# Kernel optimization log

Hardware: AMD Instinct MI355X
Metric: run time of the kernel (lower is better)

## Reference

```python
import jax, jax.numpy as jnp
import numpy as np

EMBED_DIM = 1024
NUM_HEADS = 16
HEAD_DIM = EMBED_DIM // NUM_HEADS
B, N = 8, 1024


def setup_inputs() -> dict:
    key = jax.random.key(0)
    k1, k2, k3, k4, k5, k6 = jax.random.split(key, 6)
    scale = 1.0 / np.sqrt(EMBED_DIM)
    return {
        "x": jax.random.normal(k1, (B, N, EMBED_DIM), dtype=jnp.float32),
        "attn_mask": jax.random.normal(k2, (N, N), dtype=jnp.float32) * 0.1,
        "in_proj_weight": jax.random.normal(k3, (3 * EMBED_DIM, EMBED_DIM), dtype=jnp.float32) * scale,
        "in_proj_bias": jax.random.normal(k4, (3 * EMBED_DIM,), dtype=jnp.float32) * 0.02,
        "out_w": jax.random.normal(k5, (EMBED_DIM, EMBED_DIM), dtype=jnp.float32) * scale,
        "out_b": jax.random.normal(k6, (EMBED_DIM,), dtype=jnp.float32) * 0.02,
    }


def reference(x, attn_mask, in_proj_weight, in_proj_bias, out_w, out_b):
    # x: (B, N, C); fused QKV projection as in forward_direct
    Bn, Nn, C = x.shape
    H, D = NUM_HEADS, HEAD_DIM
    qkv = x @ in_proj_weight.T + in_proj_bias            # (B, N, 3C)
    qkv = qkv.reshape(Bn, Nn, 3, H, D).transpose(2, 0, 3, 1, 4)  # (3, B, H, N, D)
    q, k, v = qkv[0], qkv[1], qkv[2]
    q = q / jnp.sqrt(jnp.asarray(D, dtype=q.dtype))
    attn = jnp.einsum("bhnd,bhmd->bhnm", q, k)           # (B, H, N, N) scores
    attn = attn + attn_mask                              # broadcast over (B, H)
    attn = jax.nn.softmax(attn, axis=-1)
    out = jnp.einsum("bhnm,bhmd->bhnd", attn, v)         # (B, H, N, D)
    out = out.transpose(0, 2, 1, 3).reshape(Bn, Nn, C)   # (B, N, C)
    return out @ out_w.T + out_b
```

## Files before the change

### kernel.cpp

```cpp
#include <hip/hip_runtime.h>


typedef __bf16 bf16x8 __attribute__((ext_vector_type(8)));
typedef float f32x4 __attribute__((ext_vector_type(4)));
typedef unsigned short us4v __attribute__((ext_vector_type(4)));

#define MFMA16 __builtin_amdgcn_mfma_f32_16x16x32_bf16

__device__ __forceinline__ unsigned short f2bf(float f) {
    return __builtin_bit_cast(unsigned short, (__bf16)f);
}

__device__ __forceinline__ us4v cvt4(float4 v) {
    us4v r;
    r.x = f2bf(v.x); r.y = f2bf(v.y); r.z = f2bf(v.z); r.w = f2bf(v.w);
    return r;
}

__device__ __forceinline__ void gl16(const unsigned short* g, unsigned short* l) {
    __builtin_amdgcn_global_load_lds(
        (const __attribute__((address_space(1))) unsigned*)g,
        (__attribute__((address_space(3))) unsigned*)l, 16, 0, 0);
}

__global__ __launch_bounds__(256)
void cvt_bf16(const float* __restrict__ src, unsigned short* __restrict__ dst,
              int n4) {
    const int i = blockIdx.x * 256 + threadIdx.x;
    if (i < n4) {
        float4 v = ((const float4*)src)[i];
        ((us4v*)dst)[i] = cvt4(v);
    }
}

__global__ __launch_bounds__(256, 3)
void qkv_gemm(const unsigned short* __restrict__ xb,
              const unsigned short* __restrict__ wb,
              const float* __restrict__ bias,
              unsigned short* __restrict__ qb, unsigned short* __restrict__ kb,
              unsigned short* __restrict__ vbT)
{
    __shared__ unsigned short lsa[2][128 * 32];
    __shared__ unsigned short lsb[2][128 * 32];
    const int tid  = threadIdx.x;
    const int wave = tid >> 6, lane = tid & 63;
    const int quad = lane >> 4, l15 = lane & 15;
    const int rch = (quad ^ ((l15 >> 1) & 3)) * 8;
    const int m0 = blockIdx.x * 128, n0 = blockIdx.y * 128;
    const int wm = (wave & 1) * 64, wn = (wave >> 1) * 64;

    const int srow = wave * 32 + (lane >> 2);
    const int scol = ((lane & 3) ^ ((lane >> 3) & 3)) * 8;
    const unsigned short* ga = xb + (size_t)(m0 + srow) * 1024 + scol;
    const unsigned short* gb = wb + (size_t)(n0 + srow) * 1024 + scol;
    const int so0 = (wave * 32) * 32;
    const int so1 = (wave * 32 + 16) * 32;

    f32x4 acc[4][4];
#pragma unroll
    for (int i = 0; i < 4; ++i)
#pragma unroll
        for (int j = 0; j < 4; ++j) acc[i][j] = (f32x4){0.f, 0.f, 0.f, 0.f};

    gl16(ga, &lsa[0][so0]);
    gl16(ga + 16 * 1024, &lsa[0][so1]);
    gl16(gb, &lsb[0][so0]);
    gl16(gb + 16 * 1024, &lsb[0][so1]);
    __syncthreads();

    int buf = 0;
    for (int kt = 0; kt < 32; ++kt) {
        if (kt < 31) {
            const int k0 = (kt + 1) * 32;
            gl16(ga + k0, &lsa[buf ^ 1][so0]);
            gl16(ga + 16 * 1024 + k0, &lsa[buf ^ 1][so1]);
            gl16(gb + k0, &lsb[buf ^ 1][so0]);
            gl16(gb + 16 * 1024 + k0, &lsb[buf ^ 1][so1]);
        }
        const unsigned short* pa = lsa[buf];
        const unsigned short* pb = lsb[buf];
        bf16x8 af[4], bfr[4];
#pragma unroll
        for (int i = 0; i < 4; ++i)
            af[i] = *(const bf16x8*)&pa[(wm + i * 16 + l15) * 32 + rch];
#pragma unroll
        for (int j = 0; j < 4; ++j)
            bfr[j] = *(const bf16x8*)&pb[(wn + j * 16 + l15) * 32 + rch];
#pragma unroll
        for (int i = 0; i < 4; ++i)
#pragma unroll
            for (int j = 0; j < 4; ++j)
                acc[i][j] = MFMA16(af[i], bfr[j], acc[i][j], 0, 0, 0);
        __syncthreads();
        buf ^= 1;
    }

    const int which = n0 >> 10;
    if (which == 2) {
#pragma unroll
        for (int j = 0; j < 4; ++j) {
            const int n = n0 + wn + j * 16 + l15;
            const int c = n & 1023;
            const int h = c >> 6, d = c & 63;
            const float bv = bias[n];
#pragma unroll
            for (int i = 0; i < 4; ++i) {
                const int m = m0 + wm + i * 16 + quad * 4;
                const int b = m >> 10, s = m & 1023;
                us4v pk;
#pragma unroll
                for (int r = 0; r < 4; ++r) pk[r] = f2bf(acc[i][j][r] + bv);
                *(us4v*)&vbT[(size_t)((b * 16 + h) * 64 + d) * 1024 + s] = pk;
            }
        }
    } else {
        unsigned short* __restrict__ dst = (which == 0) ? qb : kb;
        const float sc = (which == 0) ? 0.125f : 1.0f;
#pragma unroll
        for (int j = 0; j < 4; ++j) {
            const int n = n0 + wn + j * 16 + l15;
            const int c = n & 1023;
            const int h = c >> 6, d = c & 63;
            const float bv = bias[n];
#pragma unroll
            for (int i = 0; i < 4; ++i)
#pragma unroll
                for (int r = 0; r < 4; ++r) {
                    const int m = m0 + wm + i * 16 + quad * 4 + r;
                    const int b = m >> 10, s = m & 1023;
                    const float v = (acc[i][j][r] + bv) * sc;
                    dst[(size_t)((b * 16 + h) * 1024 + s) * 64 + d] = f2bf(v);
                }
        }
    }
}

__global__ __launch_bounds__(256, 4)
void attn_kernel(const unsigned short* __restrict__ qb,
                 const unsigned short* __restrict__ kb,
                 const unsigned short* __restrict__ vbT,
                 const float* __restrict__ mask,
                 unsigned short* __restrict__ ob)
{
    __shared__ unsigned short lsk[2][2][64 * 32];
    __shared__ unsigned short lsv[2][2][64 * 32];
    __shared__ unsigned short lsp[4][16 * 64];
    const int tid  = threadIdx.x;
    const int wave = tid >> 6, lane = tid & 63;
    const int quad = lane >> 4, l15 = lane & 15;
    const int rch = (quad ^ ((l15 >> 1) & 3)) * 8;
    const int swz = (l15 & 7) << 3;
    const int p  = blockIdx.x;
    const int lg = (p & 7) * 128 + (p >> 3);
    const int bh = lg >> 3;
    const int q0 = (lg & 7) * 128;
    const int b = bh >> 4, h = bh & 15;

    const unsigned short* __restrict__ kbase = kb + (size_t)bh * 65536;
    const unsigned short* __restrict__ vtb  = vbT + (size_t)bh * 65536;

    const int scol = ((lane & 3) ^ ((lane >> 3) & 3)) * 8;
    const unsigned short* gk = kbase + (size_t)(wave * 16 + (lane >> 2)) * 64
                                     + scol;
    const unsigned short* gv = vtb + (size_t)(wave * 16 + (lane >> 2)) * 1024
                                   + scol;
    const int so = (wave * 16) * 32;

    bf16x8 bq[2][2];
#pragma unroll
    for (int g = 0; g < 2; ++g) {
        const unsigned short* qrow =
            qb + (size_t)(bh * 1024 + q0 + wave * 32 + g * 16 + l15) * 64;
        bq[g][0] = *(const bf16x8*)(qrow + quad * 8);
        bq[g][1] = *(const bf16x8*)(qrow + 32 + quad * 8);
    }

    float lsum[2] = {0.f, 0.f};
    f32x4 oacc[2][4];
#pragma unroll
    for (int g = 0; g < 2; ++g)
#pragma unroll
        for (int nt = 0; nt < 4; ++nt) oacc[g][nt] = (f32x4){0.f, 0.f, 0.f, 0.f};

    const float* __restrict__ mrow0 =
        mask + (size_t)(q0 + wave * 32 + l15) * 1024;
    const float* __restrict__ mrow1 = mrow0 + 16 * 1024;
    unsigned short* lp = lsp[wave];

    gl16(gk, &lsk[0][0][so]);
    gl16(gk + 32, &lsk[0][1][so]);
    gl16(gv, &lsv[0][0][so]);
    gl16(gv + 32, &lsv[0][1][so]);
    __syncthreads();

    int buf = 0;
    for (int kt = 0; kt < 16; ++kt) {
        float4 mv[2][4];
#pragma unroll
        for (int nt = 0; nt < 4; ++nt) {
            mv[0][nt] = *(const float4*)&mrow0[kt * 64 + nt * 16 + quad * 4];
            mv[1][nt] = *(const float4*)&mrow1[kt * 64 + nt * 16 + quad * 4];
        }
        __builtin_amdgcn_sched_barrier(0);
        if (kt < 15) {
            gl16(gk + (size_t)(kt + 1) * 4096, &lsk[buf ^ 1][0][so]);
            gl16(gk + (size_t)(kt + 1) * 4096 + 32, &lsk[buf ^ 1][1][so]);
            gl16(gv + (size_t)(kt + 1) * 64, &lsv[buf ^ 1][0][so]);
            gl16(gv + (size_t)(kt + 1) * 64 + 32, &lsv[buf ^ 1][1][so]);
        }

        const unsigned short* rk0 = lsk[buf][0];
        const unsigned short* rk1 = lsk[buf][1];
        f32x4 s[2][4];
        __builtin_amdgcn_s_setprio(1);
#pragma unroll
        for (int nt = 0; nt < 4; ++nt) {
            const bf16x8 k0 = *(const bf16x8*)&rk0[(nt * 16 + l15) * 32 + rch];
            const bf16x8 k1 = *(const bf16x8*)&rk1[(nt * 16 + l15) * 32 + rch];
            s[0][nt] = MFMA16(k0, bq[0][0], (f32x4){0.f, 0.f, 0.f, 0.f}, 0, 0, 0);
            s[0][nt] = MFMA16(k1, bq[0][1], s[0][nt], 0, 0, 0);
            s[1][nt] = MFMA16(k0, bq[1][0], (f32x4){0.f, 0.f, 0.f, 0.f}, 0, 0, 0);
            s[1][nt] = MFMA16(k1, bq[1][1], s[1][nt], 0, 0, 0);
        }
        __builtin_amdgcn_s_setprio(0);

#pragma unroll
        for (int nt = 0; nt < 4; ++nt) {
            us4v pk;
#pragma unroll
            for (int r = 0; r < 4; ++r) {
                const float pe =
                    __expf(s[0][nt][r] + ((const float*)&mv[0][nt])[r]);
                lsum[0] += pe;
                pk[r] = f2bf(pe);
            }
            *(us4v*)&lp[(l15 << 6) + ((nt * 16 + quad * 4) ^ swz)] = pk;
        }
        bf16x8 pb0[2];
        pb0[0] = *(const bf16x8*)&lp[(l15 << 6) + ((quad * 8) ^ swz)];
        pb0[1] = *(const bf16x8*)&lp[(l15 << 6) + ((32 + quad * 8) ^ swz)];

#pragma unroll
        for (int nt = 0; nt < 4; ++nt) {
            us4v pk;
#pragma unroll
            for (int r = 0; r < 4; ++r) {
                const float pe =
                    __expf(s[1][nt][r] + ((const float*)&mv[1][nt])[r]);
                lsum[1] += pe;
                pk[r] = f2bf(pe);
            }
            *(us4v*)&lp[(l15 << 6) + ((nt * 16 + quad * 4) ^ swz)] = pk;
        }
        bf16x8 pb1[2];
        pb1[0] = *(const bf16x8*)&lp[(l15 << 6) + ((quad * 8) ^ swz)];
        pb1[1] = *(const bf16x8*)&lp[(l15 << 6) + ((32 + quad * 8) ^ swz)];

        const unsigned short* rv0 = lsv[buf][0];
        const unsigned short* rv1 = lsv[buf][1];
        __builtin_amdgcn_s_setprio(1);
#pragma unroll
        for (int nt = 0; nt < 4; ++nt) {
            const bf16x8 v0 = *(const bf16x8*)&rv0[(nt * 16 + l15) * 32 + rch];
            const bf16x8 v1 = *(const bf16x8*)&rv1[(nt * 16 + l15) * 32 + rch];
            oacc[0][nt] = MFMA16(v0, pb0[0], oacc[0][nt], 0, 0, 0);
            oacc[0][nt] = MFMA16(v1, pb0[1], oacc[0][nt], 0, 0, 0);
            oacc[1][nt] = MFMA16(v0, pb1[0], oacc[1][nt], 0, 0, 0);
            oacc[1][nt] = MFMA16(v1, pb1[1], oacc[1][nt], 0, 0, 0);
        }
        __builtin_amdgcn_s_setprio(0);

        __syncthreads();
        buf ^= 1;
    }

#pragma unroll
    for (int g = 0; g < 2; ++g) {
        lsum[g] += __shfl_xor(lsum[g], 16, 64);
        lsum[g] += __shfl_xor(lsum[g], 32, 64);
    }
#pragma unroll
    for (int g = 0; g < 2; ++g) {
        const float inv = 1.0f / lsum[g];
        unsigned short* orow =
            ob + (size_t)(b * 1024 + q0 + wave * 32 + g * 16 + l15) * 1024
               + h * 64;
#pragma unroll
        for (int nt = 0; nt < 4; ++nt) {
            us4v o;
#pragma unroll
            for (int r = 0; r < 4; ++r) o[r] = f2bf(oacc[g][nt][r] * inv);
            *(us4v*)&orow[nt * 16 + quad * 4] = o;
        }
    }
}

__global__ __launch_bounds__(256, 3)
void out_gemm(const unsigned short* __restrict__ a,
              const unsigned short* __restrict__ wb,
              const float* __restrict__ bias, float* __restrict__ out)
{
    __shared__ unsigned short lsa[2][128 * 32];
    __shared__ unsigned short lsb[2][128 * 32];
    const int tid  = threadIdx.x;
    const int wave = tid >> 6, lane = tid & 63;
    const int quad = lane >> 4, l15 = lane & 15;
    const int rch = (quad ^ ((l15 >> 1) & 3)) * 8;
    const int m0 = blockIdx.x * 128, n0 = blockIdx.y * 128;
    const int wm = (wave & 1) * 64, wn = (wave >> 1) * 64;

    const int srow = wave * 32 + (lane >> 2);
    const int scol = ((lane & 3) ^ ((lane >> 3) & 3)) * 8;
    const unsigned short* ga = a + (size_t)(m0 + srow) * 1024 + scol;
    const unsigned short* gb = wb + (size_t)(n0 + srow) * 1024 + scol;
    const int so0 = (wave * 32) * 32;
    const int so1 = (wave * 32 + 16) * 32;

    f32x4 acc[4][4];
#pragma unroll
    for (int i = 0; i < 4; ++i)
#pragma unroll
        for (int j = 0; j < 4; ++j) acc[i][j] = (f32x4){0.f, 0.f, 0.f, 0.f};

    gl16(ga, &lsa[0][so0]);
    gl16(ga + 16 * 1024, &lsa[0][so1]);
    gl16(gb, &lsb[0][so0]);
    gl16(gb + 16 * 1024, &lsb[0][so1]);
    __syncthreads();

    int buf = 0;
    for (int kt = 0; kt < 32; ++kt) {
        if (kt < 31) {
            const int k0 = (kt + 1) * 32;
            gl16(ga + k0, &lsa[buf ^ 1][so0]);
            gl16(ga + 16 * 1024 + k0, &lsa[buf ^ 1][so1]);
            gl16(gb + k0, &lsb[buf ^ 1][so0]);
            gl16(gb + 16 * 1024 + k0, &lsb[buf ^ 1][so1]);
        }
        const unsigned short* pa = lsa[buf];
        const unsigned short* pb = lsb[buf];
        bf16x8 af[4], bfr[4];
#pragma unroll
        for (int i = 0; i < 4; ++i)
            af[i] = *(const bf16x8*)&pa[(wm + i * 16 + l15) * 32 + rch];
#pragma unroll
        for (int j = 0; j < 4; ++j)
            bfr[j] = *(const bf16x8*)&pb[(wn + j * 16 + l15) * 32 + rch];
#pragma unroll
        for (int i = 0; i < 4; ++i)
#pragma unroll
            for (int j = 0; j < 4; ++j)
                acc[i][j] = MFMA16(af[i], bfr[j], acc[i][j], 0, 0, 0);
        __syncthreads();
        buf ^= 1;
    }

#pragma unroll
    for (int j = 0; j < 4; ++j) {
        const int n = n0 + wn + j * 16 + l15;
        const float bv = bias[n];
#pragma unroll
        for (int i = 0; i < 4; ++i)
#pragma unroll
            for (int r = 0; r < 4; ++r) {
                const int m = m0 + wm + i * 16 + quad * 4 + r;
                out[(size_t)m * 1024 + n] = acc[i][j][r] + bv;
            }
    }
}

extern "C" void kernel_launch(void* const* d_in, const int* in_sizes, int n_in,
                              void* d_out, int out_size, void* d_ws, size_t ws_size,
                              hipStream_t stream) {
    const float* x    = (const float*)d_in[0];
    const float* mask = (const float*)d_in[1];
    const float* win  = (const float*)d_in[2];
    const float* bin  = (const float*)d_in[3];
    const float* wout = (const float*)d_in[4];
    const float* bout = (const float*)d_in[5];
    float* out = (float*)d_out;

    char* ws = (char*)d_ws;
    unsigned short* xb = (unsigned short*)(ws);
    unsigned short* ob = (unsigned short*)(ws);
    unsigned short* qb = (unsigned short*)(ws + (size_t)(16 << 20));
    unsigned short* kb = (unsigned short*)(ws + (size_t)(32 << 20));
    unsigned short* vbT = (unsigned short*)(ws + (size_t)(48 << 20));
    unsigned short* winb  = (unsigned short*)d_out;
    unsigned short* woutb = qb;

    cvt_bf16<<<dim3(8192), 256, 0, stream>>>(x, xb, 8 * 1024 * 1024 / 4);
    cvt_bf16<<<dim3(3072), 256, 0, stream>>>(win, winb, 3 * 1024 * 1024 / 4);
    qkv_gemm<<<dim3(64, 24), 256, 0, stream>>>(xb, winb, bin, qb, kb, vbT);
    attn_kernel<<<dim3(1024), 256, 0, stream>>>(qb, kb, vbT, mask, ob);
    cvt_bf16<<<dim3(1024), 256, 0, stream>>>(wout, woutb, 1024 * 1024 / 4);
    out_gemm<<<dim3(64, 8), 256, 0, stream>>>(ob, woutb, bout, out);
}
```

Measured before the change: 302.0 us.

## Triple-buffer GEMM loads with explicit vmcnt waits; prefetch mask and split P buffers

Both projection GEMMs move from a double buffer to a three-stage LDS ring. Loads are issued two k-tiles ahead, and each stage waits with a partial vmcnt instead of a full __syncthreads drain. In the attention kernel the next tile's mask values are loaded into registers one iteration early, and each wave gets two P staging buffers so both row groups' softmax exps are computed in one pass. The end-of-iteration barrier waits on a partial vmcnt. The extra LDS and registers lower occupancy (attention launch bounds go from 4 to 3 blocks), and the hand-counted vmcnt values must exactly match the number of outstanding loads to stay correct.

```diff
diff --git a/kernel.cpp b/kernel.cpp
--- a/kernel.cpp
+++ b/kernel.cpp
@@ -40,8 +40,8 @@
               unsigned short* __restrict__ qb, unsigned short* __restrict__ kb,
               unsigned short* __restrict__ vbT)
 {
-    __shared__ unsigned short lsa[2][128 * 32];
-    __shared__ unsigned short lsb[2][128 * 32];
+    __shared__ unsigned short lsa[3][128 * 32];
+    __shared__ unsigned short lsb[3][128 * 32];
     const int tid  = threadIdx.x;
     const int wave = tid >> 6, lane = tid & 63;
     const int quad = lane >> 4, l15 = lane & 15;
@@ -66,19 +66,30 @@
     gl16(ga + 16 * 1024, &lsa[0][so1]);
     gl16(gb, &lsb[0][so0]);
     gl16(gb + 16 * 1024, &lsb[0][so1]);
-    __syncthreads();
-
-    int buf = 0;
+    gl16(ga + 32, &lsa[1][so0]);
+    gl16(ga + 16 * 1024 + 32, &lsa[1][so1]);
+    gl16(gb + 32, &lsb[1][so0]);
+    gl16(gb + 16 * 1024 + 32, &lsb[1][so1]);
+
     for (int kt = 0; kt < 32; ++kt) {
-        if (kt < 31) {
-            const int k0 = (kt + 1) * 32;
-            gl16(ga + k0, &lsa[buf ^ 1][so0]);
-            gl16(ga + 16 * 1024 + k0, &lsa[buf ^ 1][so1]);
-            gl16(gb + k0, &lsb[buf ^ 1][so0]);
-            gl16(gb + 16 * 1024 + k0, &lsb[buf ^ 1][so1]);
-        }
-        const unsigned short* pa = lsa[buf];
-        const unsigned short* pb = lsb[buf];
+        const int cb = kt % 3;
+        if (kt < 30) {
+            const int k0 = (kt + 2) * 32;
+            const int sb = (kt + 2) % 3;
+            gl16(ga + k0, &lsa[sb][so0]);
+            gl16(ga + 16 * 1024 + k0, &lsa[sb][so1]);
+            gl16(gb + k0, &lsb[sb][so0]);
+            gl16(gb + 16 * 1024 + k0, &lsb[sb][so1]);
+            asm volatile("s_waitcnt vmcnt(8)" ::: "memory");
+        } else if (kt == 30) {
+            asm volatile("s_waitcnt vmcnt(4)" ::: "memory");
+        } else {
+            asm volatile("s_waitcnt vmcnt(0)" ::: "memory");
+        }
+        __builtin_amdgcn_s_barrier();
+
+        const unsigned short* pa = lsa[cb];
+        const unsigned short* pb = lsb[cb];
         bf16x8 af[4], bfr[4];
 #pragma unroll
         for (int i = 0; i < 4; ++i)
@@ -91,8 +102,10 @@
 #pragma unroll
             for (int j = 0; j < 4; ++j)
                 acc[i][j] = MFMA16(af[i], bfr[j], acc[i][j], 0, 0, 0);
-        __syncthreads();
-        buf ^= 1;
+
+        asm volatile("s_waitcnt lgkmcnt(0)" ::: "memory");
+        __builtin_amdgcn_sched_barrier(0);
+        __builtin_amdgcn_s_barrier();
     }
 
     const int which = n0 >> 10;
@@ -135,7 +148,7 @@
     }
 }
 
-__global__ __launch_bounds__(256, 4)
+__global__ __launch_bounds__(256, 3)
 void attn_kernel(const unsigned short* __restrict__ qb,
                  const unsigned short* __restrict__ kb,
                  const unsigned short* __restrict__ vbT,
@@ -144,7 +157,7 @@
 {
     __shared__ unsigned short lsk[2][2][64 * 32];
     __shared__ unsigned short lsv[2][2][64 * 32];
-    __shared__ unsigned short lsp[4][16 * 64];
+    __shared__ unsigned short lsp[4][2][16 * 64];
     const int tid  = threadIdx.x;
     const int wave = tid >> 6, lane = tid & 63;
     const int quad = lane >> 4, l15 = lane & 15;
@@ -185,28 +198,35 @@
     const float* __restrict__ mrow0 =
         mask + (size_t)(q0 + wave * 32 + l15) * 1024;
     const float* __restrict__ mrow1 = mrow0 + 16 * 1024;
-    unsigned short* lp = lsp[wave];
 
     gl16(gk, &lsk[0][0][so]);
     gl16(gk + 32, &lsk[0][1][so]);
     gl16(gv, &lsv[0][0][so]);
     gl16(gv + 32, &lsv[0][1][so]);
+    float4 mcur[2][4];
+#pragma unroll
+    for (int nt = 0; nt < 4; ++nt) {
+        mcur[0][nt] = *(const float4*)&mrow0[nt * 16 + quad * 4];
+        mcur[1][nt] = *(const float4*)&mrow1[nt * 16 + quad * 4];
+    }
     __syncthreads();
 
     int buf = 0;
     for (int kt = 0; kt < 16; ++kt) {
-        float4 mv[2][4];
-#pragma unroll
-        for (int nt = 0; nt < 4; ++nt) {
-            mv[0][nt] = *(const float4*)&mrow0[kt * 64 + nt * 16 + quad * 4];
-            mv[1][nt] = *(const float4*)&mrow1[kt * 64 + nt * 16 + quad * 4];
-        }
-        __builtin_amdgcn_sched_barrier(0);
+        float4 mnext[2][4];
         if (kt < 15) {
             gl16(gk + (size_t)(kt + 1) * 4096, &lsk[buf ^ 1][0][so]);
             gl16(gk + (size_t)(kt + 1) * 4096 + 32, &lsk[buf ^ 1][1][so]);
             gl16(gv + (size_t)(kt + 1) * 64, &lsv[buf ^ 1][0][so]);
             gl16(gv + (size_t)(kt + 1) * 64 + 32, &lsv[buf ^ 1][1][so]);
+            __builtin_amdgcn_sched_barrier(0);
+#pragma unroll
+            for (int nt = 0; nt < 4; ++nt) {
+                mnext[0][nt] =
+                    *(const float4*)&mrow0[(kt + 1) * 64 + nt * 16 + quad * 4];
+                mnext[1][nt] =
+                    *(const float4*)&mrow1[(kt + 1) * 64 + nt * 16 + quad * 4];
+            }
         }
 
         const unsigned short* rk0 = lsk[buf][0];
@@ -224,37 +244,31 @@
         }
         __builtin_amdgcn_s_setprio(0);
 
+        unsigned short* lp0 = lsp[wave][0];
+        unsigned short* lp1 = lsp[wave][1];
 #pragma unroll
         for (int nt = 0; nt < 4; ++nt) {
-            us4v pk;
+            us4v pk0, pk1;
 #pragma unroll
             for (int r = 0; r < 4; ++r) {
-                const float pe =
-                    __expf(s[0][nt][r] + ((const float*)&mv[0][nt])[r]);
-                lsum[0] += pe;
-                pk[r] = f2bf(pe);
+                const float pe0 =
+                    __expf(s[0][nt][r] + ((const float*)&mcur[0][nt])[r]);
+                const float pe1 =
+                    __expf(s[1][nt][r] + ((const float*)&mcur[1][nt])[r]);
+                lsum[0] += pe0;
+                lsum[1] += pe1;
+                pk0[r] = f2bf(pe0);
+                pk1[r] = f2bf(pe1);
             }
-            *(us4v*)&lp[(l15 << 6) + ((nt * 16 + quad * 4) ^ swz)] = pk;
-        }
-        bf16x8 pb0[2];
-        pb0[0] = *(const bf16x8*)&lp[(l15 << 6) + ((quad * 8) ^ swz)];
-        pb0[1] = *(const bf16x8*)&lp[(l15 << 6) + ((32 + quad * 8) ^ swz)];
-
-#pragma unroll
-        for (int nt = 0; nt < 4; ++nt) {
-            us4v pk;
-#pragma unroll
-            for (int r = 0; r < 4; ++r) {
-                const float pe =
-                    __expf(s[1][nt][r] + ((const float*)&mv[1][nt])[r]);
-                lsum[1] += pe;
-                pk[r] = f2bf(pe);
-            }
-            *(us4v*)&lp[(l15 << 6) + ((nt * 16 + quad * 4) ^ swz)] = pk;
-        }
-        bf16x8 pb1[2];
-        pb1[0] = *(const bf16x8*)&lp[(l15 << 6) + ((quad * 8) ^ swz)];
-        pb1[1] = *(const bf16x8*)&lp[(l15 << 6) + ((32 + quad * 8) ^ swz)];
+            const int off = (nt * 16 + quad * 4) ^ swz;
+            *(us4v*)&lp0[(l15 << 6) + off] = pk0;
+            *(us4v*)&lp1[(l15 << 6) + off] = pk1;
+        }
+        bf16x8 pb0[2], pb1[2];
+        pb0[0] = *(const bf16x8*)&lp0[(l15 << 6) + ((quad * 8) ^ swz)];
+        pb0[1] = *(const bf16x8*)&lp0[(l15 << 6) + ((32 + quad * 8) ^ swz)];
+        pb1[0] = *(const bf16x8*)&lp1[(l15 << 6) + ((quad * 8) ^ swz)];
+        pb1[1] = *(const bf16x8*)&lp1[(l15 << 6) + ((32 + quad * 8) ^ swz)];
 
         const unsigned short* rv0 = lsv[buf][0];
         const unsigned short* rv1 = lsv[buf][1];
@@ -270,7 +284,16 @@
         }
         __builtin_amdgcn_s_setprio(0);
 
-        __syncthreads();
+        if (kt < 15) {
+            asm volatile("s_waitcnt lgkmcnt(0)" ::: "memory");
+            __builtin_amdgcn_sched_barrier(0);
+            asm volatile("s_waitcnt vmcnt(8)" ::: "memory");
+            __builtin_amdgcn_s_barrier();
+#pragma unroll
+            for (int g = 0; g < 2; ++g)
+#pragma unroll
+                for (int nt = 0; nt < 4; ++nt) mcur[g][nt] = mnext[g][nt];
+        }
         buf ^= 1;
     }
 
@@ -300,8 +323,8 @@
               const unsigned short* __restrict__ wb,
               const float* __restrict__ bias, float* __restrict__ out)
 {
-    __shared__ unsigned short lsa[2][128 * 32];
-    __shared__ unsigned short lsb[2][128 * 32];
+    __shared__ unsigned short lsa[3][128 * 32];
+    __shared__ unsigned short lsb[3][128 * 32];
     const int tid  = threadIdx.x;
     const int wave = tid >> 6, lane = tid & 63;
     const int quad = lane >> 4, l15 = lane & 15;
@@ -326,19 +349,30 @@
     gl16(ga + 16 * 1024, &lsa[0][so1]);
     gl16(gb, &lsb[0][so0]);
     gl16(gb + 16 * 1024, &lsb[0][so1]);
-    __syncthreads();
-
-    int buf = 0;
+    gl16(ga + 32, &lsa[1][so0]);
+    gl16(ga + 16 * 1024 + 32, &lsa[1][so1]);
+    gl16(gb + 32, &lsb[1][so0]);
+    gl16(gb + 16 * 1024 + 32, &lsb[1][so1]);
+
     for (int kt = 0; kt < 32; ++kt) {
-        if (kt < 31) {
-            const int k0 = (kt + 1) * 32;
-            gl16(ga + k0, &lsa[buf ^ 1][so0]);
-            gl16(ga + 16 * 1024 + k0, &lsa[buf ^ 1][so1]);
-            gl16(gb + k0, &lsb[buf ^ 1][so0]);
-            gl16(gb + 16 * 1024 + k0, &lsb[buf ^ 1][so1]);
-        }
-        const unsigned short* pa = lsa[buf];
-        const unsigned short* pb = lsb[buf];
+        const int cb = kt % 3;
+        if (kt < 30) {
+            const int k0 = (kt + 2) * 32;
+            const int sb = (kt + 2) % 3;
+            gl16(ga + k0, &lsa[sb][so0]);
+            gl16(ga + 16 * 1024 + k0, &lsa[sb][so1]);
+            gl16(gb + k0, &lsb[sb][so0]);
+            gl16(gb + 16 * 1024 + k0, &lsb[sb][so1]);
+            asm volatile("s_waitcnt vmcnt(8)" ::: "memory");
+        } else if (kt == 30) {
+            asm volatile("s_waitcnt vmcnt(4)" ::: "memory");
+        } else {
+            asm volatile("s_waitcnt vmcnt(0)" ::: "memory");
+        }
+        __builtin_amdgcn_s_barrier();
+
+        const unsigned short* pa = lsa[cb];
+        const unsigned short* pb = lsb[cb];
         bf16x8 af[4], bfr[4];
 #pragma unroll
         for (int i = 0; i < 4; ++i)
@@ -351,8 +385,10 @@
 #pragma unroll
             for (int j = 0; j < 4; ++j)
                 acc[i][j] = MFMA16(af[i], bfr[j], acc[i][j], 0, 0, 0);
-        __syncthreads();
-        buf ^= 1;
+
+        asm volatile("s_waitcnt lgkmcnt(0)" ::: "memory");
+        __builtin_amdgcn_sched_barrier(0);
+        __builtin_amdgcn_s_barrier();
     }
 
 #pragma unroll
```

New measurement: 277.3 us. -8.2%, faster.
